# Kernel tuning notes

Measured on AMD Instinct MI355X. Metric: run time of the kernel, lower is better.

The kernel has to match this reference:

```python
import jax, jax.numpy as jnp
import numpy as np

B, T, V, D, OUT = 32, 100, 10000, 128, 1000
CODE_P = 0.003  # ~30 active codes per visit


def gru_dir(x3, whh, bhh, reverse):
    """x3: [B,T,3F] precomputed input-side gates (W_ih x + b_ih). PyTorch GRU math."""
    F = whh.shape[1]
    h0 = jnp.zeros((x3.shape[0], F), x3.dtype)

    def step(h, xt):
        gh = h @ whh.T + bhh
        xr, xz, xn = jnp.split(xt, 3, -1)
        hr, hz, hn = jnp.split(gh, 3, -1)
        r = jax.nn.sigmoid(xr + hr)
        z = jax.nn.sigmoid(xz + hz)
        n = jnp.tanh(xn + r * hn)
        h_new = (1.0 - z) * n + z * h
        return h_new, h_new

    _, hs = jax.lax.scan(step, h0, jnp.swapaxes(x3, 0, 1), reverse=reverse)
    return jnp.swapaxes(hs, 0, 1)  # [B,T,F]


def setup_inputs() -> dict:
    key = jax.random.key(0)
    ks = jax.random.split(key, 16)
    s = lambda k, *sh: jax.random.normal(k, sh, dtype=jnp.float32) * 0.05
    # multi-hot visits, ~0/1 with density CODE_P; force code 0 present so no all-zero visit
    x = (jax.random.uniform(ks[0], (B, T, V)) < CODE_P).astype(jnp.float32)
    x = x.at[:, :, 0].set(1.0)
    return {
        "batchdata": x,
        "emb": s(ks[1], V, D),
        "wih_f": s(ks[2], 3 * D, D), "whh_f": s(ks[3], 3 * D, D),
        "bih_f": jnp.zeros((3 * D,), jnp.float32), "bhh_f": jnp.zeros((3 * D,), jnp.float32),
        "wih_b": s(ks[4], 3 * D, D), "whh_b": s(ks[5], 3 * D, D),
        "bih_b": jnp.zeros((3 * D,), jnp.float32), "bhh_b": jnp.zeros((3 * D,), jnp.float32),
        "attn_w": s(ks[6], 2 * D, 1), "attn_b": jnp.zeros((1,), jnp.float32),
        "comb_w": s(ks[7], D, 4 * D), "comb_b": jnp.zeros((D,), jnp.float32),
        "fc_w": s(ks[8], OUT, D), "fc_b": jnp.zeros((OUT,), jnp.float32),
    }


def reference(batchdata, emb, wih_f, whh_f, bih_f, bhh_f, wih_b, whh_b, bih_b, bhh_b,
              attn_w, attn_b, comb_w, comb_b, fc_w, fc_b):
    # multihot_to_embedding: sum of embedding rows where visit==1 == multihot @ table
    e = jnp.einsum('btv,vd->btd', batchdata, emb)          # [B,T,D]
    mask = jnp.any(e != 0, axis=2)                          # [B,T]
    # DipoleLayer: bidirectional GRU (hidden=D each dir), dropout in eval mode = identity
    xf = jnp.einsum('btf,gf->btg', e, wih_f) + bih_f
    xb = jnp.einsum('btf,gf->btg', e, wih_b) + bih_b
    hf = gru_dir(xf, whh_f, bhh_f, reverse=False)
    hb = gru_dir(xb, whh_b, bhh_b, reverse=True)
    h = jnp.concatenate([hf, hb], axis=-1)                  # [B,T,2D]
    # location-based attention over timesteps
    scores = (h @ attn_w)[..., 0] + attn_b[0]               # [B,T]
    scores = jnp.where(mask, scores, jnp.float32(-1e9))
    a = jax.nn.softmax(scores, axis=-1)
    c = jnp.einsum('bt,btf->bf', a, h)                      # [B,2D] context
    last = jnp.sum(mask.astype(jnp.int32), axis=-1) - 1     # last valid visit
    h_last = h[jnp.arange(h.shape[0]), last]                # [B,2D]
    feat = jnp.tanh(jnp.concatenate([c, h_last], -1) @ comb_w.T + comb_b)  # [B,D]
    logits = feat @ fc_w.T + fc_b                           # [B,OUT]
    return logits
```

## Files before the change

### kernel.cpp

```cpp
#include <hip/hip_runtime.h>
#include <math.h>

#define BB 32
#define TT 100
#define VV 10000
#define DD 128
#define OUTN 1000
#define G3 384

__global__ __launch_bounds__(256) void k_embed(
    const float* __restrict__ x, const float* __restrict__ emb,
    float* __restrict__ e, int* __restrict__ mask)
{
    const int bt  = blockIdx.x;
    const int tid = threadIdx.x;
    __shared__ int   s_cnt;
    __shared__ int   s_any;
    __shared__ int   s_idx[256];
    __shared__ float s_val[256];
    if (tid == 0) { s_cnt = 0; s_any = 0; }
    __syncthreads();

    const float4* x4 = (const float4*)(x + (size_t)bt * VV);
    for (int i = tid; i < VV / 4; i += 256) {
        float4 v = x4[i];
        if (v.x != 0.f) { int p = atomicAdd(&s_cnt, 1); if (p < 256) { s_idx[p] = 4*i+0; s_val[p] = v.x; } }
        if (v.y != 0.f) { int p = atomicAdd(&s_cnt, 1); if (p < 256) { s_idx[p] = 4*i+1; s_val[p] = v.y; } }
        if (v.z != 0.f) { int p = atomicAdd(&s_cnt, 1); if (p < 256) { s_idx[p] = 4*i+2; s_val[p] = v.z; } }
        if (v.w != 0.f) { int p = atomicAdd(&s_cnt, 1); if (p < 256) { s_idx[p] = 4*i+3; s_val[p] = v.w; } }
    }
    __syncthreads();
    int cnt = s_cnt; if (cnt > 256) cnt = 256;
    if (tid < DD) {
        float acc = 0.f;
        for (int i = 0; i < cnt; ++i)
            acc += s_val[i] * emb[(size_t)s_idx[i] * DD + tid];
        e[(size_t)bt * DD + tid] = acc;
        if (acc != 0.f) s_any = 1;
    }
    __syncthreads();
    if (tid == 0) mask[bt] = s_any;
}

__global__ __launch_bounds__(256) void k_gates(
    const float* __restrict__ e,
    const float* __restrict__ wih_f, const float* __restrict__ bih_f,
    const float* __restrict__ wih_b, const float* __restrict__ bih_b,
    float* __restrict__ x3)
{
    const int r0  = blockIdx.x * 8;
    const int tid = threadIdx.x;
    __shared__ __align__(16) float se[8][DD];
    for (int i = tid; i < 8 * DD; i += 256)
        se[i >> 7][i & 127] = e[(size_t)(r0 + (i >> 7)) * DD + (i & 127)];
    __syncthreads();

    for (int cc = 0; cc < 3; ++cc) {
        const int col = tid + cc * 256;
        const float* wrow;
        float bias;
        if (col < G3) { wrow = wih_f + (size_t)col * DD;        bias = bih_f[col]; }
        else          { wrow = wih_b + (size_t)(col - G3) * DD; bias = bih_b[col - G3]; }
        float acc[8];
        #pragma unroll
        for (int r = 0; r < 8; ++r) acc[r] = 0.f;
        const float4* w4 = (const float4*)wrow;
        for (int k4 = 0; k4 < DD / 4; ++k4) {
            float4 w = w4[k4];
            #pragma unroll
            for (int r = 0; r < 8; ++r) {
                float4 ev = *(const float4*)&se[r][4 * k4];
                acc[r] += ev.x * w.x + ev.y * w.y + ev.z * w.z + ev.w * w.w;
            }
        }
        #pragma unroll
        for (int r = 0; r < 8; ++r)
            x3[(size_t)(r0 + r) * 768 + col] = acc[r] + bias;
    }
}

__global__ __launch_bounds__(384) void k_gru(
    const float* __restrict__ x3,
    const float* __restrict__ whh_f, const float* __restrict__ bhh_f,
    const float* __restrict__ whh_b, const float* __restrict__ bhh_b,
    float* __restrict__ h_all)
{
    const int dir = blockIdx.x & 1;
    const int b   = blockIdx.x >> 1;
    const int g   = threadIdx.x;
    const float* whh = dir ? whh_b : whh_f;
    const float* bhh = dir ? bhh_b : bhh_f;

    float w[DD];
    const float4* wr4 = (const float4*)(whh + (size_t)g * DD);
    #pragma unroll
    for (int k4 = 0; k4 < DD / 4; ++k4) {
        float4 wv = wr4[k4];
        w[4*k4+0] = wv.x; w[4*k4+1] = wv.y; w[4*k4+2] = wv.z; w[4*k4+3] = wv.w;
    }
    const float bh = bhh[g];

    __shared__ __align__(16) float h_lds[DD];
    __shared__ float gh_lds[G3];
    float h_reg = 0.f;
    if (g < DD) h_lds[g] = 0.f;
    __syncthreads();

    for (int t = 0; t < TT; ++t) {
        const int te = dir ? (TT - 1 - t) : t;
        const float* x3p = x3 + (size_t)(b * TT + te) * 768 + dir * G3;
        float xr = 0.f, xz = 0.f, xn = 0.f;
        if (g < DD) { xr = x3p[g]; xz = x3p[DD + g]; xn = x3p[2 * DD + g]; }

        float acc = bh;
        #pragma unroll
        for (int k = 0; k < DD; k += 4) {
            float4 hv = *(const float4*)&h_lds[k];
            acc += w[k] * hv.x + w[k+1] * hv.y + w[k+2] * hv.z + w[k+3] * hv.w;
        }
        gh_lds[g] = acc;
        __syncthreads();

        if (g < DD) {
            float hr = gh_lds[g], hz = gh_lds[DD + g], hn = gh_lds[2 * DD + g];
            float r  = 1.f / (1.f + __expf(-(xr + hr)));
            float z  = 1.f / (1.f + __expf(-(xz + hz)));
            float n  = tanhf(xn + r * hn);
            float hnew = (1.f - z) * n + z * h_reg;
            h_reg = hnew;
            h_lds[g] = hnew;
            h_all[(size_t)((dir * BB + b) * TT + te) * DD + g] = hnew;
        }
        __syncthreads();
    }
}

__global__ __launch_bounds__(256) void k_attn(
    const float* __restrict__ h_all, const int* __restrict__ mask,
    const float* __restrict__ attn_w, const float* __restrict__ attn_b,
    const float* __restrict__ comb_w, const float* __restrict__ comb_b,
    float* __restrict__ feat)
{
    const int b   = blockIdx.x;
    const int tid = threadIdx.x;
    __shared__ float s_aw[256];
    __shared__ float s_sc[128];
    __shared__ int   s_m[128];
    __shared__ float s_red[128];
    __shared__ __align__(16) float s_ch[512];

    s_aw[tid] = attn_w[tid];
    int m = 0;
    if (tid < 128) {
        m = (tid < TT) ? mask[b * TT + tid] : 0;
        s_m[tid] = m;
    }
    __syncthreads();
    for (int s = 64; s > 0; s >>= 1) {
        if (tid < s) s_m[tid] += s_m[tid + s];
        __syncthreads();
    }
    const int last = s_m[0] - 1;

    const float* hf = h_all + (size_t)(0 * BB + b) * TT * DD;
    const float* hb = h_all + (size_t)(1 * BB + b) * TT * DD;

    float sc = -1e9f;
    if (tid < TT) {
        float a = attn_b[0];
        const float4* hf4 = (const float4*)(hf + (size_t)tid * DD);
        const float4* hb4 = (const float4*)(hb + (size_t)tid * DD);
        for (int k = 0; k < DD / 4; ++k) {
            float4 v = hf4[k];
            a += v.x * s_aw[4*k] + v.y * s_aw[4*k+1] + v.z * s_aw[4*k+2] + v.w * s_aw[4*k+3];
        }
        for (int k = 0; k < DD / 4; ++k) {
            float4 v = hb4[k];
            a += v.x * s_aw[DD+4*k] + v.y * s_aw[DD+4*k+1] + v.z * s_aw[DD+4*k+2] + v.w * s_aw[DD+4*k+3];
        }
        sc = m ? a : -1e9f;
    }
    if (tid < 128) { s_sc[tid] = sc; s_red[tid] = sc; }
    __syncthreads();
    for (int s = 64; s > 0; s >>= 1) {
        if (tid < s) s_red[tid] = fmaxf(s_red[tid], s_red[tid + s]);
        __syncthreads();
    }
    const float mx = s_red[0];
    __syncthreads();
    float ex = 0.f;
    if (tid < 128) { ex = __expf(s_sc[tid] - mx); s_sc[tid] = ex; s_red[tid] = ex; }
    __syncthreads();
    for (int s = 64; s > 0; s >>= 1) {
        if (tid < s) s_red[tid] += s_red[tid + s];
        __syncthreads();
    }
    const float inv = 1.f / s_red[0];
    __syncthreads();

    {
        const int fl = tid & 127;
        const float* hp = (tid < 128) ? hf : hb;
        float csum = 0.f;
        for (int t = 0; t < TT; ++t)
            csum += s_sc[t] * hp[(size_t)t * DD + fl];
        s_ch[tid]       = csum * inv;
        s_ch[256 + tid] = hp[(size_t)last * DD + fl];
    }
    __syncthreads();

    if (tid < 128) {
        float a = comb_b[tid];
        const float4* cw = (const float4*)(comb_w + (size_t)tid * 512);
        for (int k = 0; k < 128; ++k) {
            float4 w4 = cw[k];
            float4 v4 = *(const float4*)&s_ch[4 * k];
            a += w4.x * v4.x + w4.y * v4.y + w4.z * v4.z + w4.w * v4.w;
        }
        feat[(size_t)b * DD + tid] = tanhf(a);
    }
}

__global__ __launch_bounds__(256) void k_logits(
    const float* __restrict__ feat, const float* __restrict__ fc_w,
    const float* __restrict__ fc_b, float* __restrict__ out)
{
    const int b   = blockIdx.x >> 2;
    const int oc  = blockIdx.x & 3;
    const int tid = threadIdx.x;
    const int o   = oc * 256 + tid;
    __shared__ __align__(16) float s_f[DD];
    if (tid < DD) s_f[tid] = feat[(size_t)b * DD + tid];
    __syncthreads();
    if (o < OUTN) {
        float a = fc_b[o];
        const float4* w4 = (const float4*)(fc_w + (size_t)o * DD);
        for (int k = 0; k < DD / 4; ++k) {
            float4 w = w4[k];
            float4 v = *(const float4*)&s_f[4 * k];
            a += w.x * v.x + w.y * v.y + w.z * v.z + w.w * v.w;
        }
        out[(size_t)b * OUTN + o] = a;
    }
}

extern "C" void kernel_launch(void* const* d_in, const int* in_sizes, int n_in,
                              void* d_out, int out_size, void* d_ws, size_t ws_size,
                              hipStream_t stream)
{
    const float* x      = (const float*)d_in[0];
    const float* emb    = (const float*)d_in[1];
    const float* wih_f  = (const float*)d_in[2];
    const float* whh_f  = (const float*)d_in[3];
    const float* bih_f  = (const float*)d_in[4];
    const float* bhh_f  = (const float*)d_in[5];
    const float* wih_b  = (const float*)d_in[6];
    const float* whh_b  = (const float*)d_in[7];
    const float* bih_b  = (const float*)d_in[8];
    const float* bhh_b  = (const float*)d_in[9];
    const float* attn_w = (const float*)d_in[10];
    const float* attn_b = (const float*)d_in[11];
    const float* comb_w = (const float*)d_in[12];
    const float* comb_b = (const float*)d_in[13];
    const float* fc_w   = (const float*)d_in[14];
    const float* fc_b   = (const float*)d_in[15];
    float* out = (float*)d_out;

    float* ws    = (float*)d_ws;
    float* e     = ws;
    int*   mask  = (int*)(ws + 409600);
    float* x3    = ws + 412800;
    float* h_all = ws + 2870400;
    float* feat  = ws + 3689600;

    k_embed <<<BB * TT,      256, 0, stream>>>(x, emb, e, mask);
    k_gates <<<(BB * TT)/8,  256, 0, stream>>>(e, wih_f, bih_f, wih_b, bih_b, x3);
    k_gru   <<<2 * BB,       384, 0, stream>>>(x3, whh_f, bhh_f, whh_b, bhh_b, h_all);
    k_attn  <<<BB,           256, 0, stream>>>(h_all, mask, attn_w, attn_b, comb_w, comb_b, feat);
    k_logits<<<BB * 4,       256, 0, stream>>>(feat, fc_w, fc_b, out);
}
```

Baseline: 392.6 us.

## Restructure GRU recurrence, prefetch gates, fuse logits into attention, unroll embed/gates

The GRU kernel now splits each gate row's dot product across 4 lanes, with wave shuffles to reduce the partial sums. It also prefetches the next timestep's input gates, stages hidden history in LDS for one bulk store at the end, and uses a fast exp-based tanh. The logits kernel is folded into the attention kernel to save a launch and a global round-trip for feat. The embedding gather now uses four accumulators, and the gates GEMM reuses shared-memory loads across three column chunks. The aim is to shorten the serial per-step latency of the recurrence, which dominates, at the cost of more registers and 51KB of LDS per block.

```diff
diff --git a/kernel.cpp b/kernel.cpp
--- a/kernel.cpp
+++ b/kernel.cpp
@@ -32,9 +32,17 @@
     __syncthreads();
     int cnt = s_cnt; if (cnt > 256) cnt = 256;
     if (tid < DD) {
-        float acc = 0.f;
-        for (int i = 0; i < cnt; ++i)
-            acc += s_val[i] * emb[(size_t)s_idx[i] * DD + tid];
+        float a0 = 0.f, a1 = 0.f, a2 = 0.f, a3 = 0.f;
+        int i = 0;
+        for (; i + 4 <= cnt; i += 4) {
+            a0 += s_val[i+0] * emb[(size_t)s_idx[i+0] * DD + tid];
+            a1 += s_val[i+1] * emb[(size_t)s_idx[i+1] * DD + tid];
+            a2 += s_val[i+2] * emb[(size_t)s_idx[i+2] * DD + tid];
+            a3 += s_val[i+3] * emb[(size_t)s_idx[i+3] * DD + tid];
+        }
+        for (; i < cnt; ++i)
+            a0 += s_val[i] * emb[(size_t)s_idx[i] * DD + tid];
+        float acc = (a0 + a1) + (a2 + a3);
         e[(size_t)bt * DD + tid] = acc;
         if (acc != 0.f) s_any = 1;
     }
@@ -55,31 +63,43 @@
         se[i >> 7][i & 127] = e[(size_t)(r0 + (i >> 7)) * DD + (i & 127)];
     __syncthreads();
 
+    const float4* wp[3];
+    float bias[3];
+    #pragma unroll
     for (int cc = 0; cc < 3; ++cc) {
-        const int col = tid + cc * 256;
-        const float* wrow;
-        float bias;
-        if (col < G3) { wrow = wih_f + (size_t)col * DD;        bias = bih_f[col]; }
-        else          { wrow = wih_b + (size_t)(col - G3) * DD; bias = bih_b[col - G3]; }
-        float acc[8];
-        #pragma unroll
-        for (int r = 0; r < 8; ++r) acc[r] = 0.f;
-        const float4* w4 = (const float4*)wrow;
-        for (int k4 = 0; k4 < DD / 4; ++k4) {
-            float4 w = w4[k4];
+        int col = tid + cc * 256;
+        if (col < G3) { wp[cc] = (const float4*)(wih_f + (size_t)col * DD);        bias[cc] = bih_f[col]; }
+        else          { wp[cc] = (const float4*)(wih_b + (size_t)(col - G3) * DD); bias[cc] = bih_b[col - G3]; }
+    }
+
+    float acc[3][8];
+    #pragma unroll
+    for (int cc = 0; cc < 3; ++cc)
+        #pragma unroll
+        for (int r = 0; r < 8; ++r) acc[cc][r] = 0.f;
+
+    for (int k4 = 0; k4 < DD / 4; ++k4) {
+        float4 ev[8];
+        #pragma unroll
+        for (int r = 0; r < 8; ++r) ev[r] = *(const float4*)&se[r][4 * k4];
+        #pragma unroll
+        for (int cc = 0; cc < 3; ++cc) {
+            float4 w = wp[cc][k4];
             #pragma unroll
-            for (int r = 0; r < 8; ++r) {
-                float4 ev = *(const float4*)&se[r][4 * k4];
-                acc[r] += ev.x * w.x + ev.y * w.y + ev.z * w.z + ev.w * w.w;
-            }
-        }
+            for (int r = 0; r < 8; ++r)
+                acc[cc][r] += ev[r].x * w.x + ev[r].y * w.y + ev[r].z * w.z + ev[r].w * w.w;
+        }
+    }
+    #pragma unroll
+    for (int cc = 0; cc < 3; ++cc) {
+        int col = tid + cc * 256;
         #pragma unroll
         for (int r = 0; r < 8; ++r)
-            x3[(size_t)(r0 + r) * 768 + col] = acc[r] + bias;
-    }
-}
-
-__global__ __launch_bounds__(384) void k_gru(
+            x3[(size_t)(r0 + r) * 768 + col] = acc[cc][r] + bias[cc];
+    }
+}
+
+__global__ __launch_bounds__(384, 1) void k_gru(
     const float* __restrict__ x3,
     const float* __restrict__ whh_f, const float* __restrict__ bhh_f,
     const float* __restrict__ whh_b, const float* __restrict__ bhh_b,
@@ -87,59 +107,90 @@
 {
     const int dir = blockIdx.x & 1;
     const int b   = blockIdx.x >> 1;
-    const int g   = threadIdx.x;
+    const int tid = threadIdx.x;
+    const int s   = tid & 3;
+    const int rg  = tid >> 2;
     const float* whh = dir ? whh_b : whh_f;
     const float* bhh = dir ? bhh_b : bhh_f;
 
-    float w[DD];
-    const float4* wr4 = (const float4*)(whh + (size_t)g * DD);
+    float4 w4[4][8];
+    float  bh[4];
     #pragma unroll
-    for (int k4 = 0; k4 < DD / 4; ++k4) {
-        float4 wv = wr4[k4];
-        w[4*k4+0] = wv.x; w[4*k4+1] = wv.y; w[4*k4+2] = wv.z; w[4*k4+3] = wv.w;
-    }
-    const float bh = bhh[g];
-
-    __shared__ __align__(16) float h_lds[DD];
-    __shared__ float gh_lds[G3];
+    for (int j = 0; j < 4; ++j) {
+        const float4* wr = (const float4*)(whh + (size_t)(rg * 4 + j) * DD + s * 32);
+        #pragma unroll
+        for (int k4 = 0; k4 < 8; ++k4) w4[j][k4] = wr[k4];
+        bh[j] = (s == 0) ? bhh[rg * 4 + j] : 0.f;
+    }
+
+    __shared__ __align__(16) float h_pad[4 * 36];
+    __shared__ float gh[G3];
+    __shared__ __align__(16) float h_hist[TT * DD];
+
     float h_reg = 0.f;
-    if (g < DD) h_lds[g] = 0.f;
+    if (tid < 144) h_pad[tid] = 0.f;
+
+    const int g = tid;
+    const size_t xbase = (size_t)b * TT * 768 + (size_t)dir * G3;
+    float xr = 0.f, xz = 0.f, xn = 0.f;
+    if (tid < DD) {
+        const float* xp = x3 + xbase + (size_t)(dir ? TT - 1 : 0) * 768;
+        xr = xp[g]; xz = xp[DD + g]; xn = xp[2 * DD + g];
+    }
     __syncthreads();
 
     for (int t = 0; t < TT; ++t) {
-        const int te = dir ? (TT - 1 - t) : t;
-        const float* x3p = x3 + (size_t)(b * TT + te) * 768 + dir * G3;
-        float xr = 0.f, xz = 0.f, xn = 0.f;
-        if (g < DD) { xr = x3p[g]; xz = x3p[DD + g]; xn = x3p[2 * DD + g]; }
-
-        float acc = bh;
-        #pragma unroll
-        for (int k = 0; k < DD; k += 4) {
-            float4 hv = *(const float4*)&h_lds[k];
-            acc += w[k] * hv.x + w[k+1] * hv.y + w[k+2] * hv.z + w[k+3] * hv.w;
-        }
-        gh_lds[g] = acc;
-        __syncthreads();
-
-        if (g < DD) {
-            float hr = gh_lds[g], hz = gh_lds[DD + g], hn = gh_lds[2 * DD + g];
-            float r  = 1.f / (1.f + __expf(-(xr + hr)));
-            float z  = 1.f / (1.f + __expf(-(xz + hz)));
-            float n  = tanhf(xn + r * hn);
+        float nxr = 0.f, nxz = 0.f, nxn = 0.f;
+        if (tid < DD && t + 1 < TT) {
+            const float* xp = x3 + xbase + (size_t)(dir ? TT - 2 - t : t + 1) * 768;
+            nxr = xp[g]; nxz = xp[DD + g]; nxn = xp[2 * DD + g];
+        }
+
+        float a0 = bh[0], a1 = bh[1], a2 = bh[2], a3 = bh[3];
+        #pragma unroll
+        for (int k4 = 0; k4 < 8; ++k4) {
+            float4 hv = *(const float4*)&h_pad[s * 36 + 4 * k4];
+            a0 += w4[0][k4].x * hv.x + w4[0][k4].y * hv.y + w4[0][k4].z * hv.z + w4[0][k4].w * hv.w;
+            a1 += w4[1][k4].x * hv.x + w4[1][k4].y * hv.y + w4[1][k4].z * hv.z + w4[1][k4].w * hv.w;
+            a2 += w4[2][k4].x * hv.x + w4[2][k4].y * hv.y + w4[2][k4].z * hv.z + w4[2][k4].w * hv.w;
+            a3 += w4[3][k4].x * hv.x + w4[3][k4].y * hv.y + w4[3][k4].z * hv.z + w4[3][k4].w * hv.w;
+        }
+        a0 += __shfl_xor(a0, 1); a1 += __shfl_xor(a1, 1);
+        a2 += __shfl_xor(a2, 1); a3 += __shfl_xor(a3, 1);
+        a0 += __shfl_xor(a0, 2); a1 += __shfl_xor(a1, 2);
+        a2 += __shfl_xor(a2, 2); a3 += __shfl_xor(a3, 2);
+        float my = (s == 0) ? a0 : (s == 1) ? a1 : (s == 2) ? a2 : a3;
+        gh[tid] = my;
+        __syncthreads();
+
+        if (tid < DD) {
+            float hr = gh[g], hz = gh[DD + g], hn = gh[2 * DD + g];
+            float r = 1.f / (1.f + __expf(-(xr + hr)));
+            float z = 1.f / (1.f + __expf(-(xz + hz)));
+            float narg = xn + r * hn;
+            float et = __expf(-2.f * fabsf(narg));
+            float n = (1.f - et) / (1.f + et);
+            n = narg >= 0.f ? n : -n;
             float hnew = (1.f - z) * n + z * h_reg;
             h_reg = hnew;
-            h_lds[g] = hnew;
-            h_all[(size_t)((dir * BB + b) * TT + te) * DD + g] = hnew;
-        }
-        __syncthreads();
-    }
+            h_pad[(g >> 5) * 36 + (g & 31)] = hnew;
+            h_hist[(dir ? TT - 1 - t : t) * DD + g] = hnew;
+        }
+        xr = nxr; xz = nxz; xn = nxn;
+        __syncthreads();
+    }
+
+    float4* dst = (float4*)(h_all + (size_t)(dir * BB + b) * TT * DD);
+    const float4* src = (const float4*)h_hist;
+    for (int i = tid; i < TT * DD / 4; i += 384) dst[i] = src[i];
 }
 
 __global__ __launch_bounds__(256) void k_attn(
     const float* __restrict__ h_all, const int* __restrict__ mask,
     const float* __restrict__ attn_w, const float* __restrict__ attn_b,
     const float* __restrict__ comb_w, const float* __restrict__ comb_b,
-    float* __restrict__ feat)
+    const float* __restrict__ fc_w, const float* __restrict__ fc_b,
+    float* __restrict__ out)
 {
     const int b   = blockIdx.x;
     const int tid = threadIdx.x;
@@ -148,6 +199,7 @@
     __shared__ int   s_m[128];
     __shared__ float s_red[128];
     __shared__ __align__(16) float s_ch[512];
+    __shared__ __align__(16) float s_feat[DD];
 
     s_aw[tid] = attn_w[tid];
     int m = 0;
@@ -217,30 +269,21 @@
             float4 v4 = *(const float4*)&s_ch[4 * k];
             a += w4.x * v4.x + w4.y * v4.y + w4.z * v4.z + w4.w * v4.w;
         }
-        feat[(size_t)b * DD + tid] = tanhf(a);
-    }
-}
-
-__global__ __launch_bounds__(256) void k_logits(
-    const float* __restrict__ feat, const float* __restrict__ fc_w,
-    const float* __restrict__ fc_b, float* __restrict__ out)
-{
-    const int b   = blockIdx.x >> 2;
-    const int oc  = blockIdx.x & 3;
-    const int tid = threadIdx.x;
-    const int o   = oc * 256 + tid;
-    __shared__ __align__(16) float s_f[DD];
-    if (tid < DD) s_f[tid] = feat[(size_t)b * DD + tid];
-    __syncthreads();
-    if (o < OUTN) {
-        float a = fc_b[o];
+        s_feat[tid] = tanhf(a);
+    }
+    __syncthreads();
+
+    for (int o = tid; o < OUTN; o += 256) {
+        float a0 = 0.f, a1 = 0.f;
         const float4* w4 = (const float4*)(fc_w + (size_t)o * DD);
-        for (int k = 0; k < DD / 4; ++k) {
-            float4 w = w4[k];
-            float4 v = *(const float4*)&s_f[4 * k];
-            a += w.x * v.x + w.y * v.y + w.z * v.z + w.w * v.w;
-        }
-        out[(size_t)b * OUTN + o] = a;
+        #pragma unroll
+        for (int k = 0; k < DD / 8; ++k) {
+            float4 w_0 = w4[2*k],   v_0 = *(const float4*)&s_feat[8*k];
+            float4 w_1 = w4[2*k+1], v_1 = *(const float4*)&s_feat[8*k+4];
+            a0 += w_0.x * v_0.x + w_0.y * v_0.y + w_0.z * v_0.z + w_0.w * v_0.w;
+            a1 += w_1.x * v_1.x + w_1.y * v_1.y + w_1.z * v_1.z + w_1.w * v_1.w;
+        }
+        out[(size_t)b * OUTN + o] = a0 + a1 + fc_b[o];
     }
 }
 
@@ -271,11 +314,10 @@
     int*   mask  = (int*)(ws + 409600);
     float* x3    = ws + 412800;
     float* h_all = ws + 2870400;
-    float* feat  = ws + 3689600;
 
     k_embed <<<BB * TT,      256, 0, stream>>>(x, emb, e, mask);
     k_gates <<<(BB * TT)/8,  256, 0, stream>>>(e, wih_f, bih_f, wih_b, bih_b, x3);
     k_gru   <<<2 * BB,       384, 0, stream>>>(x3, whh_f, bhh_f, whh_b, bhh_b, h_all);
-    k_attn  <<<BB,           256, 0, stream>>>(h_all, mask, attn_w, attn_b, comb_w, comb_b, feat);
-    k_logits<<<BB * 4,       256, 0, stream>>>(feat, fc_w, fc_b, out);
-}
+    k_attn  <<<BB,           256, 0, stream>>>(h_all, mask, attn_w, attn_b,
+                                               comb_w, comb_b, fc_w, fc_b, out);
+}
```

Result: slower. 410.0 us (+4.4%).
